# Kernel optimization log

Hardware: AMD Instinct MI355X
Metric: run time of the kernel (lower is better)

## Reference

```python
import jax, jax.numpy as jnp
import numpy as np

HID = 128
N_NODES = 50000
N_EDGES = 800000
N_GRAPHS = 64
N_LAYERS = 2
BN_EPS = 1e-5


def setup_inputs() -> dict:
    key = jax.random.key(0)
    ks = jax.random.split(key, 12)
    x_idx = jax.random.randint(ks[0], (N_NODES,), 0, 19)
    edge_index = jax.random.randint(ks[1], (2, N_EDGES), 0, N_NODES)
    edge_attr = jax.random.randint(ks[2], (N_EDGES,), 0, 4)
    batch = jnp.sort(jax.random.randint(ks[3], (N_NODES,), 0, N_GRAPHS))
    s = 1.0 / np.sqrt(HID)
    node_emb = jax.random.normal(ks[4], (19, HID), jnp.float32)
    edge_emb = jax.random.normal(ks[5], (4, HID), jnp.float32)
    # stacked per-layer GINE MLP params: Linear->ReLU->Linear->ReLU->BN
    W1 = jax.random.uniform(ks[6], (N_LAYERS, HID, HID), jnp.float32, -s, s)
    b1 = jnp.zeros((N_LAYERS, HID), jnp.float32)
    W2 = jax.random.uniform(ks[7], (N_LAYERS, HID, HID), jnp.float32, -s, s)
    b2 = jnp.zeros((N_LAYERS, HID), jnp.float32)
    bn_g = jnp.ones((N_LAYERS, HID), jnp.float32)
    bn_b = jnp.zeros((N_LAYERS, HID), jnp.float32)
    return {"x_idx": x_idx, "edge_index": edge_index, "edge_attr": edge_attr,
            "batch": batch, "node_emb": node_emb, "edge_emb": edge_emb,
            "W1": W1, "b1": b1, "W2": W2, "b2": b2, "bn_g": bn_g, "bn_b": bn_b}


def _gine_layer(x, e_feat, src, dst, W1, b1, W2, b2, g, beta):
    # GINEConv (eps=0): nn(x + sum_{j->i} relu(x_j + e_ji))
    msg = jax.nn.relu(x[src] + e_feat)                       # [E, H] gather
    aggr = jax.ops.segment_sum(msg, dst, num_segments=x.shape[0])  # scatter-add
    h = x + aggr
    h = jax.nn.relu(h @ W1 + b1)
    h = jax.nn.relu(h @ W2 + b2)
    mu = h.mean(0)
    var = h.var(0)
    return g * (h - mu) * jax.lax.rsqrt(var + BN_EPS) + beta  # training-mode BN


def reference(x_idx, edge_index, edge_attr, batch, node_emb, edge_emb,
              W1, b1, W2, b2, bn_g, bn_b):
    x = node_emb[x_idx]                 # [N, H]
    e_feat = edge_emb[edge_attr]        # [E, H] (encoded once, shared by layers)
    src, dst = edge_index[0], edge_index[1]
    for l in range(N_LAYERS):
        x = _gine_layer(x, e_feat, src, dst, W1[l], b1[l], W2[l], b2[l], bn_g[l], bn_b[l])
    pooled = jax.ops.segment_sum(x, batch, num_segments=N_GRAPHS)  # global_add_pool
    return pooled
```

## Files before the change

### kernel.cpp

```cpp
#include <hip/hip_runtime.h>
#include <hip/hip_bf16.h>

#define HID 128
#define NNODES 50000
#define NEDGES 800000
#define NGRAPHS 64
#define BN_EPS 1e-5f
#define CAP 64

typedef __attribute__((ext_vector_type(8))) short short8;
typedef __attribute__((ext_vector_type(4))) float f32x4;

static __device__ __forceinline__ unsigned short f2bf(float v) {
  __hip_bfloat16 b = __float2bfloat16(v);
  return *reinterpret_cast<unsigned short*>(&b);
}
static __device__ __forceinline__ float bf2f(unsigned short u) {
  return __uint_as_float(((unsigned)u) << 16);
}
static __device__ __forceinline__ float lo16f(unsigned u) {
  return __uint_as_float(u << 16);
}
static __device__ __forceinline__ float hi16f(unsigned u) {
  return __uint_as_float(u & 0xFFFF0000u);
}

static __device__ __forceinline__ unsigned packhl(float v) {
  unsigned short h = f2bf(v);
  unsigned short l = f2bf(v - bf2f(h));
  return (unsigned)h | ((unsigned)l << 16);
}
static __device__ __forceinline__ float upk(unsigned p) {
  return __uint_as_float(p << 16) + __uint_as_float(p & 0xFFFF0000u);
}
static __device__ __forceinline__ void unpack8(uint4 wa, uint4 wb,
                                               short8& hi, short8& lo) {
  union U { unsigned u[4]; short8 s; };
  U H, L;
  unsigned w[8] = {wa.x, wa.y, wa.z, wa.w, wb.x, wb.y, wb.z, wb.w};
  #pragma unroll
  for (int t = 0; t < 4; t++) {
    unsigned a = w[2 * t], b = w[2 * t + 1];
    H.u[t] = (a & 0xFFFFu) | (b << 16);
    L.u[t] = (a >> 16) | (b & 0xFFFF0000u);
  }
  hi = H.s; lo = L.s;
}

__global__ __launch_bounds__(256) void prep_kernel(
    const int* __restrict__ x_idx, const float* __restrict__ node_emb,
    unsigned int* __restrict__ xb2, const int* __restrict__ eidx,
    const int* __restrict__ eattr, int* __restrict__ cnt,
    int* __restrict__ eout, const float* __restrict__ W1,
    const float* __restrict__ W2, unsigned short* __restrict__ Wpk,
    unsigned* __restrict__ msgTg, const float* __restrict__ edge_emb) {
  int i = blockIdx.x * 256 + threadIdx.x;
  int stride = gridDim.x * 256;
  const float2* ne2 = (const float2*)node_emb;
  for (int t = i; t < NNODES * (HID / 2); t += stride) {
    int n = t >> 6;
    int c2 = t & 63;
    float2 v = ne2[x_idx[n] * 64 + c2];
    xb2[t] = (unsigned)f2bf(v.x) | ((unsigned)f2bf(v.y) << 16);
  }
  for (int e = i; e < NEDGES; e += stride) {
    int s = eidx[e];
    int d = eidx[NEDGES + e];
    int ty = x_idx[s];
    int pos = atomicAdd(&cnt[d], 1);
    if (pos < CAP)
      eout[((size_t)d << 6) + pos] = s | (eattr[e] << 16) | (ty << 18);
  }
  for (int idx = i; idx < 76 * 64; idx += stride) {
    int combo = idx >> 6, c2 = (idx & 63) << 1;
    int ty = combo >> 2, at = combo & 3;
    float a0 = fmaxf(node_emb[ty * HID + c2] + edge_emb[at * HID + c2], 0.f);
    float a1 = fmaxf(node_emb[ty * HID + c2 + 1] + edge_emb[at * HID + c2 + 1], 0.f);
    msgTg[idx] = (unsigned)f2bf(a0) | ((unsigned)f2bf(a1) << 16);
  }
  for (int idx = i; idx < 65536; idx += stride) {
    int j = idx & 7;
    int l = (idx >> 3) & 63;
    int q = (idx >> 9) & 3;
    int t = (idx >> 11) & 7;
    int m = idx >> 14;
    int k = ((l >> 4) << 3) + j + (q << 5);
    int n = (t << 4) + (l & 15);
    int layer = m >> 1;
    const float* W = (m & 1) ? W2 : W1;
    float w = W[(size_t)layer * HID * HID + k * HID + n];
    unsigned short h = f2bf(w);
    Wpk[idx] = h;
    Wpk[idx + 65536] = f2bf(w - bf2f(h));
  }
}

#define NT 48
#define LDAF 132
#define GRID_GINE ((NNODES + NT - 1) / NT)

template <bool L0>
__global__ __launch_bounds__(512, 8) void gine_mlp_kernel(
    const unsigned short* __restrict__ in_bf,
    const float* __restrict__ instats,
    const float* __restrict__ gam, const float* __restrict__ bet,
    const int* __restrict__ cnt, const int* __restrict__ eout,
    const unsigned* __restrict__ msgTg, const float* __restrict__ edge_emb,
    const short8* __restrict__ Wh, const short8* __restrict__ Wl,
    const float* __restrict__ b1, const float* __restrict__ b2,
    unsigned short* __restrict__ out_bf, float* __restrict__ stats,
    const int* __restrict__ batch, float* __restrict__ gpool) {
  extern __shared__ __align__(16) char smem[];
  unsigned* hAp = (unsigned*)smem;
  float* sheL = (float*)(smem + NT * LDAF * 4);
  float* red = (float*)(smem + NT * LDAF * 4);

  const int tid = threadIdx.x;
  const int lane = tid & 63;
  const int wave = tid >> 6;
  const int base = blockIdx.x * NT;

  float scl_lo = 1.0f, scl_hi = 1.0f, sh_lo = 0.0f, sh_hi = 0.0f;

  if constexpr (!L0) {
    if (tid < 4 * HID) {
      int c = tid & 127;
      float mu = instats[c] * (1.0f / NNODES);
      float var = instats[HID + c] * (1.0f / NNODES) - mu * mu;
      float s = gam[c] * rsqrtf(var + BN_EPS);
      float shc = bet[c] - mu * s;
      sheL[tid] = shc + edge_emb[tid];
    }
    {
      int c0 = lane << 1;
      float mu0 = instats[c0] * (1.0f / NNODES);
      float var0 = instats[HID + c0] * (1.0f / NNODES) - mu0 * mu0;
      scl_lo = gam[c0] * rsqrtf(var0 + BN_EPS);
      sh_lo = bet[c0] - mu0 * scl_lo;
      float mu1 = instats[c0 + 1] * (1.0f / NNODES);
      float var1 = instats[HID + c0 + 1] * (1.0f / NNODES) - mu1 * mu1;
      scl_hi = gam[c0 + 1] * rsqrtf(var1 + BN_EPS);
      sh_hi = bet[c0 + 1] - mu1 * scl_hi;
    }
    __syncthreads();
  }

  {
    const unsigned* in4 = (const unsigned*)in_bf;
    int node0 = base + wave * 6;
    float acc0[6], acc1[6];
    #pragma unroll
    for (int i = 0; i < 6; i++) { acc0[i] = 0.0f; acc1[i] = 0.0f; }

    int dg6[6], epw6[6];
    unsigned sv6[6];
    #pragma unroll
    for (int i = 0; i < 6; i++) {
      int node = node0 + i;
      bool v = node < NNODES;
      dg6[i] = v ? __builtin_amdgcn_readfirstlane(min(cnt[node], CAP)) : 0;
      epw6[i] = v ? eout[(node << 6) + lane] : 0;
      sv6[i] = v ? in4[(node << 6) + lane] : 0u;
    }

#define GL_ISSUE(SB, X, A)                                      \
    {                                                           \
      _Pragma("unroll")                                         \
      for (int jj = 0; jj < 8; jj++) {                          \
        if ((SB) + jj < dg) {                                   \
          int w = __builtin_amdgcn_readlane(epw, (SB) + jj);    \
          A[jj] = (w >> 16) & 3;                                \
          X[jj] = in4[((w & 0xFFFF) << 6) + lane];              \
        }                                                       \
      }                                                         \
    }
#define GL_CONS(SB, X, A)                                       \
    {                                                           \
      _Pragma("unroll")                                         \
      for (int jj = 0; jj < 8; jj++) {                          \
        if ((SB) + jj < dg) {                                   \
          float2 e2 = *(const float2*)&sheL[(A[jj] << 7) + (lane << 1)]; \
          acc0[i] += fmaxf(fmaf(lo16f(X[jj]), scl_lo, e2.x), 0.0f); \
          acc1[i] += fmaxf(fmaf(hi16f(X[jj]), scl_hi, e2.y), 0.0f); \
        }                                                       \
      }                                                         \
    }
#define GT_ISSUE(SB, M)                                         \
    {                                                           \
      _Pragma("unroll")                                         \
      for (int jj = 0; jj < 8; jj++) {                          \
        if ((SB) + jj < dg) {                                   \
          int w = __builtin_amdgcn_readlane(epw, (SB) + jj);    \
          M[jj] = msgTg[(((w >> 16) & 127) << 6) + lane];       \
        }                                                       \
      }                                                         \
    }
#define GT_CONS(SB, M)                                          \
    {                                                           \
      _Pragma("unroll")                                         \
      for (int jj = 0; jj < 8; jj++) {                          \
        if ((SB) + jj < dg) {                                   \
          acc0[i] += lo16f(M[jj]);                              \
          acc1[i] += hi16f(M[jj]);                              \
        }                                                       \
      }                                                         \
    }

    #pragma unroll
    for (int i = 0; i < 6; i++) {
      int node = node0 + i;
      if (node >= NNODES) continue;
      int dg = dg6[i];
      int epw = epw6[i];
      if constexpr (L0) {
        acc0[i] = lo16f(sv6[i]);
        acc1[i] = hi16f(sv6[i]);
      } else {
        acc0[i] = fmaf(lo16f(sv6[i]), scl_lo, sh_lo);
        acc1[i] = fmaf(hi16f(sv6[i]), scl_hi, sh_hi);
      }
      if (dg > 0) {
        if constexpr (L0) {
          unsigned M0[8], M1[8];
          GT_ISSUE(0, M0);
          int s = 0;
          for (;;) {
            if (s * 8 + 8 < dg) GT_ISSUE(s * 8 + 8, M1);
            GT_CONS(s * 8, M0);
            s++;
            if (s * 8 >= dg) break;
            if (s * 8 + 8 < dg) GT_ISSUE(s * 8 + 8, M0);
            GT_CONS(s * 8, M1);
            s++;
            if (s * 8 >= dg) break;
          }
        } else {
          unsigned X0[8], X1[8];
          int A0[8], A1[8];
          GL_ISSUE(0, X0, A0);
          int s = 0;
          for (;;) {
            if (s * 8 + 8 < dg) GL_ISSUE(s * 8 + 8, X1, A1);
            GL_CONS(s * 8, X0, A0);
            s++;
            if (s * 8 >= dg) break;
            if (s * 8 + 8 < dg) GL_ISSUE(s * 8 + 8, X0, A0);
            GL_CONS(s * 8, X1, A1);
            s++;
            if (s * 8 >= dg) break;
          }
        }
      }
    }
#undef GL_ISSUE
#undef GL_CONS
#undef GT_ISSUE
#undef GT_CONS

    #pragma unroll
    for (int i = 0; i < 6; i++) {
      int nrow = wave * 6 + i;
      hAp[nrow * LDAF + (lane << 1)] = packhl(acc0[i]);
      hAp[nrow * LDAF + (lane << 1) + 1] = packhl(acc1[i]);
    }
  }
  __syncthreads();

  const int col = lane & 15;
  const int quad = lane >> 4;
  const int rbase = quad * 4;
  const int ch0 = wave * 16 + col;
  const int aoff = quad * 8;

  {
    f32x4 a0 = {0.f, 0.f, 0.f, 0.f}, a1 = a0, a2 = a0;
    #pragma unroll
    for (int q = 0; q < 4; q++) {
      int f0 = wave * 256 + q * 64 + lane;
      short8 b0h = Wh[f0], b0l = Wl[f0];
      const unsigned* r0 = &hAp[col * LDAF + q * 32 + aoff];
      const unsigned* r1 = &hAp[(16 + col) * LDAF + q * 32 + aoff];
      const unsigned* r2 = &hAp[(32 + col) * LDAF + q * 32 + aoff];
      short8 a0h, a0l, a1h, a1l, a2h, a2l;
      unpack8(*(const uint4*)r0, *(const uint4*)(r0 + 4), a0h, a0l);
      unpack8(*(const uint4*)r1, *(const uint4*)(r1 + 4), a1h, a1l);
      unpack8(*(const uint4*)r2, *(const uint4*)(r2 + 4), a2h, a2l);
      a0 = __builtin_amdgcn_mfma_f32_16x16x32_bf16(a0h, b0h, a0, 0, 0, 0);
      a0 = __builtin_amdgcn_mfma_f32_16x16x32_bf16(a0l, b0h, a0, 0, 0, 0);
      a0 = __builtin_amdgcn_mfma_f32_16x16x32_bf16(a0h, b0l, a0, 0, 0, 0);
      a1 = __builtin_amdgcn_mfma_f32_16x16x32_bf16(a1h, b0h, a1, 0, 0, 0);
      a1 = __builtin_amdgcn_mfma_f32_16x16x32_bf16(a1l, b0h, a1, 0, 0, 0);
      a1 = __builtin_amdgcn_mfma_f32_16x16x32_bf16(a1h, b0l, a1, 0, 0, 0);
      a2 = __builtin_amdgcn_mfma_f32_16x16x32_bf16(a2h, b0h, a2, 0, 0, 0);
      a2 = __builtin_amdgcn_mfma_f32_16x16x32_bf16(a2l, b0h, a2, 0, 0, 0);
      a2 = __builtin_amdgcn_mfma_f32_16x16x32_bf16(a2h, b0l, a2, 0, 0, 0);
    }
    __syncthreads();
    float bb0 = b1[ch0];
    #pragma unroll
    for (int r = 0; r < 4; r++) {
      hAp[(rbase + r) * LDAF + ch0] = packhl(fmaxf(a0[r] + bb0, 0.0f));
      hAp[(16 + rbase + r) * LDAF + ch0] = packhl(fmaxf(a1[r] + bb0, 0.0f));
      hAp[(32 + rbase + r) * LDAF + ch0] = packhl(fmaxf(a2[r] + bb0, 0.0f));
    }
  }
  __syncthreads();

  {
    f32x4 a0 = {0.f, 0.f, 0.f, 0.f}, a1 = a0, a2 = a0;
    #pragma unroll
    for (int q = 0; q < 4; q++) {
      int f0 = 2048 + wave * 256 + q * 64 + lane;
      short8 b0h = Wh[f0], b0l = Wl[f0];
      const unsigned* r0 = &hAp[col * LDAF + q * 32 + aoff];
      const unsigned* r1 = &hAp[(16 + col) * LDAF + q * 32 + aoff];
      const unsigned* r2 = &hAp[(32 + col) * LDAF + q * 32 + aoff];
      short8 a0h, a0l, a1h, a1l, a2h, a2l;
      unpack8(*(const uint4*)r0, *(const uint4*)(r0 + 4), a0h, a0l);
      unpack8(*(const uint4*)r1, *(const uint4*)(r1 + 4), a1h, a1l);
      unpack8(*(const uint4*)r2, *(const uint4*)(r2 + 4), a2h, a2l);
      a0 = __builtin_amdgcn_mfma_f32_16x16x32_bf16(a0h, b0h, a0, 0, 0, 0);
      a0 = __builtin_amdgcn_mfma_f32_16x16x32_bf16(a0l, b0h, a0, 0, 0, 0);
      a0 = __builtin_amdgcn_mfma_f32_16x16x32_bf16(a0h, b0l, a0, 0, 0, 0);
      a1 = __builtin_amdgcn_mfma_f32_16x16x32_bf16(a1h, b0h, a1, 0, 0, 0);
      a1 = __builtin_amdgcn_mfma_f32_16x16x32_bf16(a1l, b0h, a1, 0, 0, 0);
      a1 = __builtin_amdgcn_mfma_f32_16x16x32_bf16(a1h, b0l, a1, 0, 0, 0);
      a2 = __builtin_amdgcn_mfma_f32_16x16x32_bf16(a2h, b0h, a2, 0, 0, 0);
      a2 = __builtin_amdgcn_mfma_f32_16x16x32_bf16(a2l, b0h, a2, 0, 0, 0);
      a2 = __builtin_amdgcn_mfma_f32_16x16x32_bf16(a2h, b0l, a2, 0, 0, 0);
    }
    __syncthreads();
    float bb0 = b2[ch0];
    #pragma unroll
    for (int r = 0; r < 4; r++) {
      hAp[(rbase + r) * LDAF + ch0] = packhl(fmaxf(a0[r] + bb0, 0.0f));
      hAp[(16 + rbase + r) * LDAF + ch0] = packhl(fmaxf(a1[r] + bb0, 0.0f));
      hAp[(32 + rbase + r) * LDAF + ch0] = packhl(fmaxf(a2[r] + bb0, 0.0f));
    }
  }
  __syncthreads();

  float lsum = 0.0f, lsq = 0.0f;
  if (tid < 256) {
    const int c = tid & 127;
    const int yy = tid >> 7;
    if (out_bf) {
      #pragma unroll 4
      for (int i = 0; i < 24; i++) {
        int n = yy * 24 + i;
        int node = base + n;
        if (node < NNODES) {
          unsigned p = hAp[n * LDAF + c];
          out_bf[node * HID + c] = (unsigned short)(p & 0xFFFF);
          float v = upk(p);
          lsum += v;
          lsq += v * v;
        }
      }
    } else {
      int curg = -1;
      float pacc = 0.0f;
      for (int i = 0; i < 24; i++) {
        int n = yy * 24 + i;
        int node = base + n;
        if (node < NNODES) {
          float v = upk(hAp[n * LDAF + c]);
          lsum += v;
          lsq += v * v;
          int bg = batch[node];
          if (bg != curg) {
            if (curg >= 0) unsafeAtomicAdd(&gpool[curg * HID + c], pacc);
            curg = bg;
            pacc = 0.0f;
          }
          pacc += v;
        }
      }
      if (curg >= 0) unsafeAtomicAdd(&gpool[curg * HID + c], pacc);
    }
    if (tid >= 128) {
      red[tid - 128] = lsum;
      red[tid] = lsq;
    }
  }
  __syncthreads();
  if (tid < 128) {
    lsum += red[tid];
    lsq += red[128 + tid];
    unsafeAtomicAdd(&stats[tid], lsum);
    unsafeAtomicAdd(&stats[HID + tid], lsq);
  }
}

__device__ __forceinline__ int lbound(const int* __restrict__ arr, int n,
                                      int key) {
  int lo = 0, hi = n;
  while (lo < hi) {
    int mid = (lo + hi) >> 1;
    if (arr[mid] < key) lo = mid + 1; else hi = mid;
  }
  return lo;
}

__global__ __launch_bounds__(128) void finish_kernel(
    const float* __restrict__ gpool, const float* __restrict__ stats,
    const float* __restrict__ gam, const float* __restrict__ bet,
    const int* __restrict__ batch, float* __restrict__ out) {
  __shared__ int cnt_s;
  int g = blockIdx.x, c = threadIdx.x;
  if (c == 0)
    cnt_s = lbound(batch, NNODES, g + 1) - lbound(batch, NNODES, g);
  __syncthreads();
  float mu = stats[c] * (1.0f / NNODES);
  float var = stats[HID + c] * (1.0f / NNODES) - mu * mu;
  float scl = gam[c] * rsqrtf(var + BN_EPS);
  float sh = bet[c] - mu * scl;
  out[g * HID + c] = fmaf(gpool[g * HID + c], scl, (float)cnt_s * sh);
}

extern "C" void kernel_launch(void* const* d_in, const int* in_sizes, int n_in,
                              void* d_out, int out_size, void* d_ws, size_t ws_size,
                              hipStream_t stream) {
  const int* x_idx = (const int*)d_in[0];
  const int* eidx = (const int*)d_in[1];
  const int* eattr = (const int*)d_in[2];
  const int* batch = (const int*)d_in[3];
  const float* node_emb = (const float*)d_in[4];
  const float* edge_emb = (const float*)d_in[5];
  const float* W1 = (const float*)d_in[6];
  const float* b1 = (const float*)d_in[7];
  const float* W2 = (const float*)d_in[8];
  const float* b2 = (const float*)d_in[9];
  const float* bn_g = (const float*)d_in[10];
  const float* bn_b = (const float*)d_in[11];
  float* out = (float*)d_out;

  const size_t nfeat = (size_t)NNODES * HID;
  unsigned short* xbf = (unsigned short*)d_ws;
  unsigned short* h2bf = xbf + nfeat;
  float* stats0 = (float*)(h2bf + nfeat);
  float* stats1 = stats0 + 2 * HID;
  float* gpool = stats1 + 2 * HID;
  int* cnt = (int*)(gpool + NGRAPHS * HID);
  int* eout = cnt + NNODES;
  unsigned short* Wpk = (unsigned short*)(eout + (size_t)NNODES * CAP);
  unsigned* msgTg = (unsigned*)(Wpk + 131072);
  size_t needed = (size_t)((char*)(msgTg + 76 * 64) - (char*)d_ws);
  if (ws_size < needed) return;

  hipMemsetAsync(stats0, 0, (4 * HID + NGRAPHS * HID + NNODES) * sizeof(int),
                 stream);

  prep_kernel<<<1024, 256, 0, stream>>>(x_idx, node_emb, (unsigned int*)xbf,
                                        eidx, eattr, cnt, eout, W1, W2, Wpk,
                                        msgTg, edge_emb);

  const short8* Wfh = (const short8*)Wpk;
  const short8* Wfl = Wfh + 8192;
  const size_t smemsz = (size_t)NT * LDAF * 4 + 4 * HID * 4;
  gine_mlp_kernel<true><<<GRID_GINE, 512, smemsz, stream>>>(
      xbf, nullptr, nullptr, nullptr, cnt, eout, msgTg, edge_emb,
      Wfh + 0 * 2048, Wfl + 0 * 2048, b1, b2, h2bf, stats0, nullptr, nullptr);
  gine_mlp_kernel<false><<<GRID_GINE, 512, smemsz, stream>>>(
      h2bf, stats0, bn_g, bn_b, cnt, eout, msgTg, edge_emb,
      Wfh + 2 * 2048, Wfl + 2 * 2048, b1 + HID, b2 + HID, nullptr, stats1,
      batch, gpool);
  finish_kernel<<<NGRAPHS, 128, 0, stream>>>(gpool, stats1, bn_g + HID,
                                             bn_b + HID, batch, out);
}
```

Before: 302.4 us.

## Drop materialized node embedding; shrink node tile to 32 per block

Removes the prep pass that wrote a bf16 copy of the embedded node features for all nodes. Layer 0 now reads the self term from a small 19-row type table indexed by x_idx, so a full N×H write and read is avoided. The node tile per block also drops from 48 to 32 (4 nodes per wave, two MFMA row groups instead of three), and launch bounds change to a lower minimum block count. This gives more, smaller blocks, at the cost of reusing each weight fetch across fewer rows.

```diff
diff --git a/kernel.cpp b/kernel.cpp
--- a/kernel.cpp
+++ b/kernel.cpp
@@ -49,20 +49,13 @@
 
 __global__ __launch_bounds__(256) void prep_kernel(
     const int* __restrict__ x_idx, const float* __restrict__ node_emb,
-    unsigned int* __restrict__ xb2, const int* __restrict__ eidx,
-    const int* __restrict__ eattr, int* __restrict__ cnt,
-    int* __restrict__ eout, const float* __restrict__ W1,
-    const float* __restrict__ W2, unsigned short* __restrict__ Wpk,
-    unsigned* __restrict__ msgTg, const float* __restrict__ edge_emb) {
+    const int* __restrict__ eidx, const int* __restrict__ eattr,
+    int* __restrict__ cnt, int* __restrict__ eout,
+    const float* __restrict__ W1, const float* __restrict__ W2,
+    unsigned short* __restrict__ Wpk, unsigned* __restrict__ msgTg,
+    unsigned* __restrict__ typeT, const float* __restrict__ edge_emb) {
   int i = blockIdx.x * 256 + threadIdx.x;
   int stride = gridDim.x * 256;
-  const float2* ne2 = (const float2*)node_emb;
-  for (int t = i; t < NNODES * (HID / 2); t += stride) {
-    int n = t >> 6;
-    int c2 = t & 63;
-    float2 v = ne2[x_idx[n] * 64 + c2];
-    xb2[t] = (unsigned)f2bf(v.x) | ((unsigned)f2bf(v.y) << 16);
-  }
   for (int e = i; e < NEDGES; e += stride) {
     int s = eidx[e];
     int d = eidx[NEDGES + e];
@@ -77,6 +70,11 @@
     float a0 = fmaxf(node_emb[ty * HID + c2] + edge_emb[at * HID + c2], 0.f);
     float a1 = fmaxf(node_emb[ty * HID + c2 + 1] + edge_emb[at * HID + c2 + 1], 0.f);
     msgTg[idx] = (unsigned)f2bf(a0) | ((unsigned)f2bf(a1) << 16);
+  }
+  for (int idx = i; idx < 19 * 64; idx += stride) {
+    int ty = idx >> 6, c2 = (idx & 63) << 1;
+    typeT[idx] = (unsigned)f2bf(node_emb[ty * HID + c2]) |
+                 ((unsigned)f2bf(node_emb[ty * HID + c2 + 1]) << 16);
   }
   for (int idx = i; idx < 65536; idx += stride) {
     int j = idx & 7;
@@ -95,13 +93,14 @@
   }
 }
 
-#define NT 48
+#define NT 32
 #define LDAF 132
 #define GRID_GINE ((NNODES + NT - 1) / NT)
 
 template <bool L0>
-__global__ __launch_bounds__(512, 8) void gine_mlp_kernel(
+__global__ __launch_bounds__(512, 4) void gine_mlp_kernel(
     const unsigned short* __restrict__ in_bf,
+    const int* __restrict__ xidx,
     const float* __restrict__ instats,
     const float* __restrict__ gam, const float* __restrict__ bet,
     const int* __restrict__ cnt, const int* __restrict__ eout,
@@ -147,20 +146,25 @@
 
   {
     const unsigned* in4 = (const unsigned*)in_bf;
-    int node0 = base + wave * 6;
-    float acc0[6], acc1[6];
-    #pragma unroll
-    for (int i = 0; i < 6; i++) { acc0[i] = 0.0f; acc1[i] = 0.0f; }
-
-    int dg6[6], epw6[6];
-    unsigned sv6[6];
-    #pragma unroll
-    for (int i = 0; i < 6; i++) {
+    int node0 = base + wave * 4;
+    float acc0[4], acc1[4];
+    #pragma unroll
+    for (int i = 0; i < 4; i++) { acc0[i] = 0.0f; acc1[i] = 0.0f; }
+
+    int dg4[4], epw4[4];
+    unsigned sv4[4];
+    #pragma unroll
+    for (int i = 0; i < 4; i++) {
       int node = node0 + i;
       bool v = node < NNODES;
-      dg6[i] = v ? __builtin_amdgcn_readfirstlane(min(cnt[node], CAP)) : 0;
-      epw6[i] = v ? eout[(node << 6) + lane] : 0;
-      sv6[i] = v ? in4[(node << 6) + lane] : 0u;
+      dg4[i] = v ? __builtin_amdgcn_readfirstlane(min(cnt[node], CAP)) : 0;
+      epw4[i] = v ? eout[(node << 6) + lane] : 0;
+      int srow;
+      if constexpr (L0)
+        srow = v ? __builtin_amdgcn_readfirstlane(xidx[node]) : 0;
+      else
+        srow = node;
+      sv4[i] = v ? in4[(srow << 6) + lane] : 0u;
     }
 
 #define GL_ISSUE(SB, X, A)                                      \
@@ -207,17 +211,17 @@
     }
 
     #pragma unroll
-    for (int i = 0; i < 6; i++) {
+    for (int i = 0; i < 4; i++) {
       int node = node0 + i;
       if (node >= NNODES) continue;
-      int dg = dg6[i];
-      int epw = epw6[i];
+      int dg = dg4[i];
+      int epw = epw4[i];
       if constexpr (L0) {
-        acc0[i] = lo16f(sv6[i]);
-        acc1[i] = hi16f(sv6[i]);
+        acc0[i] = lo16f(sv4[i]);
+        acc1[i] = hi16f(sv4[i]);
       } else {
-        acc0[i] = fmaf(lo16f(sv6[i]), scl_lo, sh_lo);
-        acc1[i] = fmaf(hi16f(sv6[i]), scl_hi, sh_hi);
+        acc0[i] = fmaf(lo16f(sv4[i]), scl_lo, sh_lo);
+        acc1[i] = fmaf(hi16f(sv4[i]), scl_hi, sh_hi);
       }
       if (dg > 0) {
         if constexpr (L0) {
@@ -258,8 +262,8 @@
 #undef GT_CONS
 
     #pragma unroll
-    for (int i = 0; i < 6; i++) {
-      int nrow = wave * 6 + i;
+    for (int i = 0; i < 4; i++) {
+      int nrow = wave * 4 + i;
       hAp[nrow * LDAF + (lane << 1)] = packhl(acc0[i]);
       hAp[nrow * LDAF + (lane << 1) + 1] = packhl(acc1[i]);
     }
@@ -273,27 +277,22 @@
   const int aoff = quad * 8;
 
   {
-    f32x4 a0 = {0.f, 0.f, 0.f, 0.f}, a1 = a0, a2 = a0;
+    f32x4 a0 = {0.f, 0.f, 0.f, 0.f}, a1 = a0;
     #pragma unroll
     for (int q = 0; q < 4; q++) {
       int f0 = wave * 256 + q * 64 + lane;
       short8 b0h = Wh[f0], b0l = Wl[f0];
       const unsigned* r0 = &hAp[col * LDAF + q * 32 + aoff];
       const unsigned* r1 = &hAp[(16 + col) * LDAF + q * 32 + aoff];
-      const unsigned* r2 = &hAp[(32 + col) * LDAF + q * 32 + aoff];
-      short8 a0h, a0l, a1h, a1l, a2h, a2l;
+      short8 a0h, a0l, a1h, a1l;
       unpack8(*(const uint4*)r0, *(const uint4*)(r0 + 4), a0h, a0l);
       unpack8(*(const uint4*)r1, *(const uint4*)(r1 + 4), a1h, a1l);
-      unpack8(*(const uint4*)r2, *(const uint4*)(r2 + 4), a2h, a2l);
       a0 = __builtin_amdgcn_mfma_f32_16x16x32_bf16(a0h, b0h, a0, 0, 0, 0);
       a0 = __builtin_amdgcn_mfma_f32_16x16x32_bf16(a0l, b0h, a0, 0, 0, 0);
       a0 = __builtin_amdgcn_mfma_f32_16x16x32_bf16(a0h, b0l, a0, 0, 0, 0);
       a1 = __builtin_amdgcn_mfma_f32_16x16x32_bf16(a1h, b0h, a1, 0, 0, 0);
       a1 = __builtin_amdgcn_mfma_f32_16x16x32_bf16(a1l, b0h, a1, 0, 0, 0);
       a1 = __builtin_amdgcn_mfma_f32_16x16x32_bf16(a1h, b0l, a1, 0, 0, 0);
-      a2 = __builtin_amdgcn_mfma_f32_16x16x32_bf16(a2h, b0h, a2, 0, 0, 0);
-      a2 = __builtin_amdgcn_mfma_f32_16x16x32_bf16(a2l, b0h, a2, 0, 0, 0);
-      a2 = __builtin_amdgcn_mfma_f32_16x16x32_bf16(a2h, b0l, a2, 0, 0, 0);
     }
     __syncthreads();
     float bb0 = b1[ch0];
@@ -301,33 +300,27 @@
     for (int r = 0; r < 4; r++) {
       hAp[(rbase + r) * LDAF + ch0] = packhl(fmaxf(a0[r] + bb0, 0.0f));
       hAp[(16 + rbase + r) * LDAF + ch0] = packhl(fmaxf(a1[r] + bb0, 0.0f));
-      hAp[(32 + rbase + r) * LDAF + ch0] = packhl(fmaxf(a2[r] + bb0, 0.0f));
     }
   }
   __syncthreads();
 
   {
-    f32x4 a0 = {0.f, 0.f, 0.f, 0.f}, a1 = a0, a2 = a0;
+    f32x4 a0 = {0.f, 0.f, 0.f, 0.f}, a1 = a0;
     #pragma unroll
     for (int q = 0; q < 4; q++) {
       int f0 = 2048 + wave * 256 + q * 64 + lane;
       short8 b0h = Wh[f0], b0l = Wl[f0];
       const unsigned* r0 = &hAp[col * LDAF + q * 32 + aoff];
       const unsigned* r1 = &hAp[(16 + col) * LDAF + q * 32 + aoff];
-      const unsigned* r2 = &hAp[(32 + col) * LDAF + q * 32 + aoff];
-      short8 a0h, a0l, a1h, a1l, a2h, a2l;
+      short8 a0h, a0l, a1h, a1l;
       unpack8(*(const uint4*)r0, *(const uint4*)(r0 + 4), a0h, a0l);
       unpack8(*(const uint4*)r1, *(const uint4*)(r1 + 4), a1h, a1l);
-      unpack8(*(const uint4*)r2, *(const uint4*)(r2 + 4), a2h, a2l);
       a0 = __builtin_amdgcn_mfma_f32_16x16x32_bf16(a0h, b0h, a0, 0, 0, 0);
       a0 = __builtin_amdgcn_mfma_f32_16x16x32_bf16(a0l, b0h, a0, 0, 0, 0);
       a0 = __builtin_amdgcn_mfma_f32_16x16x32_bf16(a0h, b0l, a0, 0, 0, 0);
       a1 = __builtin_amdgcn_mfma_f32_16x16x32_bf16(a1h, b0h, a1, 0, 0, 0);
       a1 = __builtin_amdgcn_mfma_f32_16x16x32_bf16(a1l, b0h, a1, 0, 0, 0);
       a1 = __builtin_amdgcn_mfma_f32_16x16x32_bf16(a1h, b0l, a1, 0, 0, 0);
-      a2 = __builtin_amdgcn_mfma_f32_16x16x32_bf16(a2h, b0h, a2, 0, 0, 0);
-      a2 = __builtin_amdgcn_mfma_f32_16x16x32_bf16(a2l, b0h, a2, 0, 0, 0);
-      a2 = __builtin_amdgcn_mfma_f32_16x16x32_bf16(a2h, b0l, a2, 0, 0, 0);
     }
     __syncthreads();
     float bb0 = b2[ch0];
@@ -335,7 +328,6 @@
     for (int r = 0; r < 4; r++) {
       hAp[(rbase + r) * LDAF + ch0] = packhl(fmaxf(a0[r] + bb0, 0.0f));
       hAp[(16 + rbase + r) * LDAF + ch0] = packhl(fmaxf(a1[r] + bb0, 0.0f));
-      hAp[(32 + rbase + r) * LDAF + ch0] = packhl(fmaxf(a2[r] + bb0, 0.0f));
     }
   }
   __syncthreads();
@@ -346,8 +338,8 @@
     const int yy = tid >> 7;
     if (out_bf) {
       #pragma unroll 4
-      for (int i = 0; i < 24; i++) {
-        int n = yy * 24 + i;
+      for (int i = 0; i < 16; i++) {
+        int n = yy * 16 + i;
         int node = base + n;
         if (node < NNODES) {
           unsigned p = hAp[n * LDAF + c];
@@ -360,8 +352,8 @@
     } else {
       int curg = -1;
       float pacc = 0.0f;
-      for (int i = 0; i < 24; i++) {
-        int n = yy * 24 + i;
+      for (int i = 0; i < 16; i++) {
+        int n = yy * 16 + i;
         int node = base + n;
         if (node < NNODES) {
           float v = upk(hAp[n * LDAF + c]);
@@ -436,8 +428,7 @@
   float* out = (float*)d_out;
 
   const size_t nfeat = (size_t)NNODES * HID;
-  unsigned short* xbf = (unsigned short*)d_ws;
-  unsigned short* h2bf = xbf + nfeat;
+  unsigned short* h2bf = (unsigned short*)d_ws;
   float* stats0 = (float*)(h2bf + nfeat);
   float* stats1 = stats0 + 2 * HID;
   float* gpool = stats1 + 2 * HID;
@@ -445,24 +436,26 @@
   int* eout = cnt + NNODES;
   unsigned short* Wpk = (unsigned short*)(eout + (size_t)NNODES * CAP);
   unsigned* msgTg = (unsigned*)(Wpk + 131072);
-  size_t needed = (size_t)((char*)(msgTg + 76 * 64) - (char*)d_ws);
+  unsigned* typeT = msgTg + 76 * 64;
+  size_t needed = (size_t)((char*)(typeT + 19 * 64) - (char*)d_ws);
   if (ws_size < needed) return;
 
   hipMemsetAsync(stats0, 0, (4 * HID + NGRAPHS * HID + NNODES) * sizeof(int),
                  stream);
 
-  prep_kernel<<<1024, 256, 0, stream>>>(x_idx, node_emb, (unsigned int*)xbf,
-                                        eidx, eattr, cnt, eout, W1, W2, Wpk,
-                                        msgTg, edge_emb);
+  prep_kernel<<<1024, 256, 0, stream>>>(x_idx, node_emb, eidx, eattr, cnt,
+                                        eout, W1, W2, Wpk, msgTg, typeT,
+                                        edge_emb);
 
   const short8* Wfh = (const short8*)Wpk;
   const short8* Wfl = Wfh + 8192;
   const size_t smemsz = (size_t)NT * LDAF * 4 + 4 * HID * 4;
   gine_mlp_kernel<true><<<GRID_GINE, 512, smemsz, stream>>>(
-      xbf, nullptr, nullptr, nullptr, cnt, eout, msgTg, edge_emb,
-      Wfh + 0 * 2048, Wfl + 0 * 2048, b1, b2, h2bf, stats0, nullptr, nullptr);
+      (const unsigned short*)typeT, x_idx, nullptr, nullptr, nullptr, cnt,
+      eout, msgTg, edge_emb, Wfh + 0 * 2048, Wfl + 0 * 2048, b1, b2, h2bf,
+      stats0, nullptr, nullptr);
   gine_mlp_kernel<false><<<GRID_GINE, 512, smemsz, stream>>>(
-      h2bf, stats0, bn_g, bn_b, cnt, eout, msgTg, edge_emb,
+      h2bf, nullptr, stats0, bn_g, bn_b, cnt, eout, msgTg, edge_emb,
       Wfh + 2 * 2048, Wfl + 2 * 2048, b1 + HID, b2 + HID, nullptr, stats1,
       batch, gpool);
   finish_kernel<<<NGRAPHS, 128, 0, stream>>>(gpool, stats1, bn_g + HID,
```

After: 275.3 us. -9.0%, faster.
